# Optimization experiments

Hardware: AMD Instinct MI355X
Metric: run time of the kernel (lower is better)

Reference implementation:

```python
import jax, jax.numpy as jnp
import numpy as np

BS, T, F, D_IN, NH, D_OUT = 8, 32, 128, 64, 8, 64
GAUSS_STD = 2.0


def setup_inputs() -> dict:
    key = jax.random.key(0)
    ks = jax.random.split(key, 9)
    X = jax.random.normal(ks[0], (BS, F, T, D_IN), dtype=jnp.float32)
    W_query = jax.random.normal(ks[1], (T, F, D_IN, NH, 2), dtype=jnp.float32)
    W_key = jax.random.normal(ks[2], (T, F, D_IN, NH, 2), dtype=jnp.float32)
    Wkey_ = jax.random.normal(ks[3], (T, 2, 2), dtype=jnp.float32)
    u = jax.random.normal(ks[4], (T, F, 2), dtype=jnp.float32)
    attention_center = GAUSS_STD * jax.random.normal(ks[5], (T, NH, 1), dtype=jnp.float32)
    alpha = jax.random.normal(ks[6], (T,), dtype=jnp.float32)
    # relative position features: [F, F, 2] = (delta^2, delta), tiled over T
    rel = (jnp.arange(F)[None, :] - jnp.arange(F)[:, None]).astype(jnp.float32)
    R = jnp.broadcast_to(jnp.stack([rel ** 2, rel], axis=-1)[None], (T, F, F, 2))
    W = jax.random.normal(ks[7], (T, NH * D_IN, D_OUT), dtype=jnp.float32)
    b = jax.random.normal(ks[8], (F, T, D_OUT), dtype=jnp.float32)
    return {"X": X, "W_query": W_query, "W_key": W_key, "Wkey_": Wkey_,
            "u": u, "attention_center": attention_center, "alpha": alpha,
            "R": R, "W": W, "b": b}


def reference(X, W_query, W_key, Wkey_, u, attention_center, alpha, R, W, b):
    # X: [bs, F, T, d_in] -> [bs, T, F, d_in]
    Xp = jnp.transpose(X, (0, 2, 1, 3))
    bs = Xp.shape[0]
    query = jnp.einsum('btfd,tfdhe->btfhe', Xp, W_query)  # [bs,T,F,Nh,2]
    key_t = jnp.einsum('btfd,tfdhe->btfhe', Xp, W_key)    # [bs,T,F,Nh,2]
    r_delta = jnp.einsum('tde,tfle->tfld', Wkey_, R)      # [T,F,F,2]
    centers = jnp.concatenate([jnp.ones_like(attention_center),
                               -2.0 * attention_center], axis=-1)  # [T,Nh,2]
    v = -alpha[:, None, None] * centers                   # [T,Nh,2]
    scores = (jnp.einsum('btfhe,btlhe->btfhl', query, key_t)
              + jnp.einsum('btfhe,tfle->btfhl', query, r_delta)
              + jnp.einsum('tle,btfhe->btfhl', u, key_t)
              + jnp.einsum('the,tfle->tfhl', v, r_delta)[None])  # [bs,T,F,Nh,F]
    probs = jax.nn.softmax(scores, axis=-1)
    vals = jnp.einsum('btfhl,btld->btfhd', probs, Xp)     # [bs,T,F,Nh,d_in]
    vals = vals.reshape(bs, T, F, NH * D_IN)
    out = jnp.einsum('btfd,tdo->bfto', vals, W) + b[None]  # [bs,F,T,d_out]
    return out
```

## Files before the change

kernel.cpp:

```cpp
#include <hip/hip_runtime.h>
#include <hip/hip_bf16.h>

#define NBS 8
#define NT 32
#define NF 128
#define NDIN 64
#define NNH 8
#define NDOUT 64

typedef __bf16 bf16_t;
typedef __bf16 bf16x8 __attribute__((ext_vector_type(8)));
typedef float f32x4 __attribute__((ext_vector_type(4)));
typedef float f32x2 __attribute__((ext_vector_type(2)));

__global__ __launch_bounds__(256, 4)
void qk_project_kernel(const float* __restrict__ X,
                       const float* __restrict__ Wq,
                       const float* __restrict__ Wk,
                       float* __restrict__ q_ws,
                       float* __restrict__ k_ws)
{
    __shared__ float lx[4][8][64];
    const int w = threadIdx.x >> 6, lane = threadIdx.x & 63;
    const int gw = blockIdx.x * 4 + w;
    const int t = gw >> 7, f = gw & 127;

    {
        const int b = lane >> 3, d8 = (lane & 7) << 3;
        const float* src = &X[(((size_t)b * NF + f) * NT + t) * NDIN + d8];
        const float4 v0 = *(const float4*)src;
        const float4 v1 = *(const float4*)(src + 4);
        *(float4*)&lx[w][b][d8]     = v0;
        *(float4*)&lx[w][b][d8 + 4] = v1;
    }
    __syncthreads();

    const int dq = lane >> 4, he = lane & 15;
    const float* wq = Wq + ((size_t)t * NF + f) * (NDIN * 16);
    const float* wk = Wk + ((size_t)t * NF + f) * (NDIN * 16);
    float qa[8] = {0,0,0,0,0,0,0,0}, ka[8] = {0,0,0,0,0,0,0,0};
    for (int d0 = 0; d0 < NDIN; d0 += 4) {
        const int d = d0 + dq;
        const float wqv = wq[d * 16 + he];
        const float wkv = wk[d * 16 + he];
#pragma unroll
        for (int b = 0; b < 8; ++b) {
            const float x = lx[w][b][d];
            qa[b] = fmaf(x, wqv, qa[b]);
            ka[b] = fmaf(x, wkv, ka[b]);
        }
    }
#pragma unroll
    for (int b = 0; b < 8; ++b) {
        qa[b] += __shfl_xor(qa[b], 16); qa[b] += __shfl_xor(qa[b], 32);
        ka[b] += __shfl_xor(ka[b], 16); ka[b] += __shfl_xor(ka[b], 32);
    }
#pragma unroll
    for (int bb = 0; bb < 2; ++bb) {
        const int b = dq + bb * 4;
        q_ws[(((size_t)b * NT + t) * 16 + he) * NF + f] = qa[b];
        k_ws[(((size_t)b * NT + t) * 16 + he) * NF + f] = ka[b];
    }
}

__global__ __launch_bounds__(512, 2)
void spatial_attn_kernel(const float* __restrict__ X,
                         const float* __restrict__ q_ws,
                         const float* __restrict__ k_ws,
                         const float* __restrict__ Wkey,
                         const float* __restrict__ U,
                         const float* __restrict__ AC,
                         const float* __restrict__ Alpha,
                         const float* __restrict__ Wo,
                         const float* __restrict__ Bias,
                         float* __restrict__ Out)
{
    const int blk  = blockIdx.x;
    const int b    = blk & 7;
    const int t    = blk >> 3;
    const int tid  = threadIdx.x;
    const int w    = tid >> 6;
    const int lane = tid & 63;
    const int cq   = lane & 15;
    const int rq   = lane >> 4;
    const int rt   = w;
    const int frow = 16 * rt + cq;

    __shared__ __align__(16) unsigned char smem[75776];
    bf16_t* XTs   = (bf16_t*)smem;
    float*  kvh   = (float*)(smem + 16384);
    float*  kvu   = (float*)(smem + 24576);
    float4 (*qf)[128] = (float4 (*)[128])(smem + 25600);
    bf16_t* WTs   = (bf16_t*)(smem + 41984);
    bf16_t (*Vscr)[16][68] = (bf16_t (*)[16][68])(smem + 58368);

#pragma unroll
    for (int r = 0; r < 4; ++r) {
        const int idx = tid + r * 512;
        const int f = idx >> 4, d4 = (idx & 15) << 2;
        const float4 v = *(const float4*)&X[(((size_t)b * NF + f) * NT + t) * NDIN + d4];
        float vv[4]; vv[0] = v.x; vv[1] = v.y; vv[2] = v.z; vv[3] = v.w;
#pragma unroll
        for (int i = 0; i < 4; ++i) {
            const int d = d4 + i;
            XTs[d * 128 + (((f >> 3) ^ (d & 15)) << 3) + (f & 7)] = (bf16_t)vv[i];
        }
    }
#pragma unroll
    for (int r = 0; r < 2; ++r) {
        const int idx = tid + r * 512;
        const int hh = idx >> 7, l = idx & 127;
        const size_t qkb = ((size_t)b * NT + t) * 16;
        const float k0 = k_ws[(qkb + 2 * hh + 0) * NF + l];
        const float k1 = k_ws[(qkb + 2 * hh + 1) * NF + l];
        const float q0 = q_ws[(qkb + 2 * hh + 0) * NF + l];
        const float q1 = q_ws[(qkb + 2 * hh + 1) * NF + l];
        qf[hh][l] = make_float4(q0, q1, k0, k1);
        const int P = l >> 1, c = l & 1;
        const int base = (hh * 64 + P) * 4;
        kvh[base + 0 + c] = k0;
        kvh[base + 2 + c] = k1;
    }
    if (tid < 128) {
        const int l = tid;
        const float2 u01 = *(const float2*)&U[((size_t)t * NF + l) * 2];
        const int P = l >> 1, c = l & 1;
        kvu[P * 4 + 0 + c] = u01.x;
        kvu[P * 4 + 2 + c] = u01.y;
    }
#pragma unroll
    for (int r = 0; r < 2; ++r) {
        const int idx = tid + r * 512;
        const int dd = idx >> 4, o4 = (idx & 15) << 2;
        const float4 v = *(const float4*)&Wo[((size_t)t * 512 + dd) * NDOUT + o4];
        float vv[4]; vv[0] = v.x; vv[1] = v.y; vv[2] = v.z; vv[3] = v.w;
#pragma unroll
        for (int i = 0; i < 4; ++i) {
            const int o = o4 + i;
            WTs[o * 64 + (((dd >> 3) ^ (o & 7)) << 3) + (dd & 7)] = (bf16_t)vv[i];
        }
    }

    const float alpha_t = Alpha[t];
    const float wk00 = Wkey[t * 4 + 0], wk01 = Wkey[t * 4 + 1];
    const float wk10 = Wkey[t * 4 + 2], wk11 = Wkey[t * 4 + 3];

    __syncthreads();

    f32x4 oacc[4] = { {0.f,0.f,0.f,0.f}, {0.f,0.f,0.f,0.f}, {0.f,0.f,0.f,0.f}, {0.f,0.f,0.f,0.f} };

#pragma unroll 1
    for (int h = 0; h < NNH; ++h) {
        if (h < 7) {
            const int bn = ((h + 1) & 1) * 4096;
#pragma unroll
            for (int r = 0; r < 2; ++r) {
                const int idx = tid + r * 512;
                const int dd = idx >> 4, o4 = (idx & 15) << 2;
                const float4 v = *(const float4*)&Wo[((size_t)t * 512 + (h + 1) * 64 + dd) * NDOUT + o4];
                float vv[4]; vv[0] = v.x; vv[1] = v.y; vv[2] = v.z; vv[3] = v.w;
#pragma unroll
                for (int i = 0; i < 4; ++i) {
                    const int o = o4 + i;
                    WTs[bn + o * 64 + (((dd >> 3) ^ (o & 7)) << 3) + (dd & 7)] = (bf16_t)vv[i];
                }
            }
        }
        const int buf = (h & 1) * 4096;
        const float4 qq = qf[h][frow];
        const float q0 = qq.x, q1 = qq.y, kf0 = qq.z, kf1 = qq.w;
        const float v1 = 2.f * alpha_t * AC[t * NNH + h];
        const float c0 = (q0 - alpha_t) * wk00 + (q1 + v1) * wk10;
        const float c1 = (q0 - alpha_t) * wk01 + (q1 + v1) * wk11;

        f32x2 sc2[4][4];
        f32x2 mx2 = { -3.0e38f, -3.0e38f };
#pragma unroll
        for (int kt = 0; kt < 4; ++kt) {
#pragma unroll
            for (int j2 = 0; j2 < 4; ++j2) {
                const int P = kt * 16 + rq * 4 + j2;
                const float4 kp = *(const float4*)&kvh[(h * 64 + P) * 4];
                const float4 up = *(const float4*)&kvu[P * 4];
                const f32x2 k0p = { kp.x, kp.y };
                const f32x2 k1p = { kp.z, kp.w };
                const f32x2 u0p = { up.x, up.y };
                const f32x2 u1p = { up.z, up.w };
                const float l0 = (float)(kt * 32 + rq * 8 + 2 * j2 - frow);
                const f32x2 delp = { l0, l0 + 1.f };
                f32x2 sv = k0p * q0 + k1p * q1 + u0p * kf0 + u1p * kf1
                         + (delp * c0 + c1) * delp;
                sc2[kt][j2] = sv;
                mx2 = __builtin_elementwise_max(mx2, sv);
            }
        }
        float rowmax = fmaxf(mx2.x, mx2.y);
        rowmax = fmaxf(rowmax, __shfl_xor(rowmax, 16));
        rowmax = fmaxf(rowmax, __shfl_xor(rowmax, 32));
        f32x2 s2 = { 0.f, 0.f };
#pragma unroll
        for (int kt = 0; kt < 4; ++kt)
#pragma unroll
            for (int j2 = 0; j2 < 4; ++j2) {
                f32x2 sv = sc2[kt][j2];
                const f32x2 e = { __expf(sv.x - rowmax), __expf(sv.y - rowmax) };
                s2 += e;
                sc2[kt][j2] = e;
            }
        float sum = s2.x + s2.y;
        sum += __shfl_xor(sum, 16);
        sum += __shfl_xor(sum, 32);
        const float rinv = 1.f / sum;

        f32x4 vacc[4] = { {0.f,0.f,0.f,0.f}, {0.f,0.f,0.f,0.f}, {0.f,0.f,0.f,0.f}, {0.f,0.f,0.f,0.f} };
#pragma unroll
        for (int kt = 0; kt < 4; ++kt) {
            bf16x8 pf;
#pragma unroll
            for (int j2 = 0; j2 < 4; ++j2) {
                const f32x2 e = sc2[kt][j2];
                pf[2 * j2 + 0] = (bf16_t)(e.x * rinv);
                pf[2 * j2 + 1] = (bf16_t)(e.y * rinv);
            }
#pragma unroll
            for (int ct = 0; ct < 4; ++ct) {
                const bf16x8 bb = *(const bf16x8*)&XTs[(ct * 16 + cq) * 128 + (((kt * 4 + rq) ^ cq) << 3)];
                vacc[ct] = __builtin_amdgcn_mfma_f32_16x16x32_bf16(pf, bb, vacc[ct], 0, 0, 0);
            }
        }
#pragma unroll
        for (int ct = 0; ct < 4; ++ct)
#pragma unroll
            for (int rr = 0; rr < 4; ++rr)
                Vscr[w][rq * 4 + rr][ct * 16 + cq] = (bf16_t)vacc[ct][rr];

#pragma unroll
        for (int kt = 0; kt < 2; ++kt) {
            const bf16x8 a = *(const bf16x8*)&Vscr[w][cq][kt * 32 + rq * 8];
#pragma unroll
            for (int ct = 0; ct < 4; ++ct) {
                const bf16x8 bw = *(const bf16x8*)&WTs[buf + (ct * 16 + cq) * 64 + (((kt * 4 + rq) ^ (cq & 7)) << 3)];
                oacc[ct] = __builtin_amdgcn_mfma_f32_16x16x32_bf16(a, bw, oacc[ct], 0, 0, 0);
            }
        }
        __syncthreads();
    }

#pragma unroll
    for (int ct = 0; ct < 4; ++ct) {
#pragma unroll
        for (int rr = 0; rr < 4; ++rr) {
            const int f = 16 * rt + rq * 4 + rr;
            const int o = ct * 16 + cq;
            Out[(((size_t)b * NF + f) * NT + t) * NDOUT + o] =
                oacc[ct][rr] + Bias[((size_t)f * NT + t) * NDOUT + o];
        }
    }
}

extern "C" void kernel_launch(void* const* d_in, const int* in_sizes, int n_in,
                              void* d_out, int out_size, void* d_ws, size_t ws_size,
                              hipStream_t stream) {
    (void)in_sizes; (void)n_in; (void)ws_size; (void)out_size;
    const float* X    = (const float*)d_in[0];
    const float* Wq   = (const float*)d_in[1];
    const float* Wk   = (const float*)d_in[2];
    const float* Wkey = (const float*)d_in[3];
    const float* U    = (const float*)d_in[4];
    const float* AC   = (const float*)d_in[5];
    const float* Al   = (const float*)d_in[6];
    const float* Wo   = (const float*)d_in[8];
    const float* Bias = (const float*)d_in[9];

    float* q_ws = (float*)d_ws;
    float* k_ws = q_ws + (size_t)NBS * NT * 16 * NF;

    qk_project_kernel<<<dim3(NT * NF / 4), dim3(256), 0, stream>>>(X, Wq, Wk, q_ws, k_ws);
    spatial_attn_kernel<<<dim3(NBS * NT), dim3(512), 0, stream>>>(
        X, q_ws, k_ws, Wkey, U, AC, Al, Wo, Bias, (float*)d_out);
}
```

Before: 52.24 us.

## Preload all head output weights into LDS and hoist X and u fragments to registers

All eight heads' slices of the output projection weight are now staged in shared memory before the head loop, which removes the per-head double-buffered reload and the per-iteration __syncthreads. The X transposed fragments and the u coefficients, which do not change across heads, are loaded once into registers instead of being re-read from LDS every head. LDS use rises to about 122 KB per block, which likely limits occupancy to one block per CU. The hoisted arrays also add roughly 100 VGPRs of pressure.

```diff
diff --git a/kernel.cpp b/kernel.cpp
--- a/kernel.cpp
+++ b/kernel.cpp
@@ -86,13 +86,13 @@
     const int rt   = w;
     const int frow = 16 * rt + cq;
 
-    __shared__ __align__(16) unsigned char smem[75776];
+    __shared__ __align__(16) unsigned char smem[124928];
     bf16_t* XTs   = (bf16_t*)smem;
     float*  kvh   = (float*)(smem + 16384);
     float*  kvu   = (float*)(smem + 24576);
     float4 (*qf)[128] = (float4 (*)[128])(smem + 25600);
-    bf16_t* WTs   = (bf16_t*)(smem + 41984);
-    bf16_t (*Vscr)[16][68] = (bf16_t (*)[16][68])(smem + 58368);
+    bf16_t* WTall = (bf16_t*)(smem + 41984);
+    bf16_t (*Vscr)[16][68] = (bf16_t (*)[16][68])(smem + 107520);
 
 #pragma unroll
     for (int r = 0; r < 4; ++r) {
@@ -129,15 +129,16 @@
         kvu[P * 4 + 2 + c] = u01.y;
     }
 #pragma unroll
-    for (int r = 0; r < 2; ++r) {
-        const int idx = tid + r * 512;
-        const int dd = idx >> 4, o4 = (idx & 15) << 2;
-        const float4 v = *(const float4*)&Wo[((size_t)t * 512 + dd) * NDOUT + o4];
+    for (int rep = 0; rep < 16; ++rep) {
+        const int flat = rep * 512 + tid;
+        const int h = flat >> 10, f10 = flat & 1023;
+        const int dd = f10 >> 4, o4 = (f10 & 15) << 2;
+        const float4 v = *(const float4*)&Wo[((size_t)t * 512 + h * 64 + dd) * NDOUT + o4];
         float vv[4]; vv[0] = v.x; vv[1] = v.y; vv[2] = v.z; vv[3] = v.w;
 #pragma unroll
         for (int i = 0; i < 4; ++i) {
             const int o = o4 + i;
-            WTs[o * 64 + (((dd >> 3) ^ (o & 7)) << 3) + (dd & 7)] = (bf16_t)vv[i];
+            WTall[h * 4096 + o * 64 + (((dd >> 3) ^ (o & 7)) << 3) + (dd & 7)] = (bf16_t)vv[i];
         }
     }
 
@@ -147,26 +148,28 @@
 
     __syncthreads();
 
+    bf16x8 xreg[4][4];
+#pragma unroll
+    for (int kt = 0; kt < 4; ++kt)
+#pragma unroll
+        for (int ct = 0; ct < 4; ++ct)
+            xreg[kt][ct] = *(const bf16x8*)&XTs[(ct * 16 + cq) * 128 + (((kt * 4 + rq) ^ cq) << 3)];
+
+    f32x2 u0r[4][4], u1r[4][4];
+#pragma unroll
+    for (int kt = 0; kt < 4; ++kt)
+#pragma unroll
+        for (int j2 = 0; j2 < 4; ++j2) {
+            const int P = kt * 16 + rq * 4 + j2;
+            const float4 up = *(const float4*)&kvu[P * 4];
+            u0r[kt][j2] = (f32x2){ up.x, up.y };
+            u1r[kt][j2] = (f32x2){ up.z, up.w };
+        }
+
     f32x4 oacc[4] = { {0.f,0.f,0.f,0.f}, {0.f,0.f,0.f,0.f}, {0.f,0.f,0.f,0.f}, {0.f,0.f,0.f,0.f} };
 
 #pragma unroll 1
     for (int h = 0; h < NNH; ++h) {
-        if (h < 7) {
-            const int bn = ((h + 1) & 1) * 4096;
-#pragma unroll
-            for (int r = 0; r < 2; ++r) {
-                const int idx = tid + r * 512;
-                const int dd = idx >> 4, o4 = (idx & 15) << 2;
-                const float4 v = *(const float4*)&Wo[((size_t)t * 512 + (h + 1) * 64 + dd) * NDOUT + o4];
-                float vv[4]; vv[0] = v.x; vv[1] = v.y; vv[2] = v.z; vv[3] = v.w;
-#pragma unroll
-                for (int i = 0; i < 4; ++i) {
-                    const int o = o4 + i;
-                    WTs[bn + o * 64 + (((dd >> 3) ^ (o & 7)) << 3) + (dd & 7)] = (bf16_t)vv[i];
-                }
-            }
-        }
-        const int buf = (h & 1) * 4096;
         const float4 qq = qf[h][frow];
         const float q0 = qq.x, q1 = qq.y, kf0 = qq.z, kf1 = qq.w;
         const float v1 = 2.f * alpha_t * AC[t * NNH + h];
@@ -181,14 +184,11 @@
             for (int j2 = 0; j2 < 4; ++j2) {
                 const int P = kt * 16 + rq * 4 + j2;
                 const float4 kp = *(const float4*)&kvh[(h * 64 + P) * 4];
-                const float4 up = *(const float4*)&kvu[P * 4];
                 const f32x2 k0p = { kp.x, kp.y };
                 const f32x2 k1p = { kp.z, kp.w };
-                const f32x2 u0p = { up.x, up.y };
-                const f32x2 u1p = { up.z, up.w };
                 const float l0 = (float)(kt * 32 + rq * 8 + 2 * j2 - frow);
                 const f32x2 delp = { l0, l0 + 1.f };
-                f32x2 sv = k0p * q0 + k1p * q1 + u0p * kf0 + u1p * kf1
+                f32x2 sv = k0p * q0 + k1p * q1 + u0r[kt][j2] * kf0 + u1r[kt][j2] * kf1
                          + (delp * c0 + c1) * delp;
                 sc2[kt][j2] = sv;
                 mx2 = __builtin_elementwise_max(mx2, sv);
@@ -223,10 +223,8 @@
                 pf[2 * j2 + 1] = (bf16_t)(e.y * rinv);
             }
 #pragma unroll
-            for (int ct = 0; ct < 4; ++ct) {
-                const bf16x8 bb = *(const bf16x8*)&XTs[(ct * 16 + cq) * 128 + (((kt * 4 + rq) ^ cq) << 3)];
-                vacc[ct] = __builtin_amdgcn_mfma_f32_16x16x32_bf16(pf, bb, vacc[ct], 0, 0, 0);
-            }
+            for (int ct = 0; ct < 4; ++ct)
+                vacc[ct] = __builtin_amdgcn_mfma_f32_16x16x32_bf16(pf, xreg[kt][ct], vacc[ct], 0, 0, 0);
         }
 #pragma unroll
         for (int ct = 0; ct < 4; ++ct)
@@ -239,11 +237,10 @@
             const bf16x8 a = *(const bf16x8*)&Vscr[w][cq][kt * 32 + rq * 8];
 #pragma unroll
             for (int ct = 0; ct < 4; ++ct) {
-                const bf16x8 bw = *(const bf16x8*)&WTs[buf + (ct * 16 + cq) * 64 + (((kt * 4 + rq) ^ (cq & 7)) << 3)];
+                const bf16x8 bw = *(const bf16x8*)&WTall[h * 4096 + (ct * 16 + cq) * 64 + (((kt * 4 + rq) ^ (cq & 7)) << 3)];
                 oacc[ct] = __builtin_amdgcn_mfma_f32_16x16x32_bf16(a, bw, oacc[ct], 0, 0, 0);
             }
         }
-        __syncthreads();
     }
 
 #pragma unroll
```

Result: faster. 47.59 us (-8.9%).
